# Performance work log

Hardware: AMD Instinct MI355X
Metric: run time of the kernel (lower is better)

The kernel has to match this reference:

```python
import jax, jax.numpy as jnp
import numpy as np

SOS = 1
V, H, B, T = 32000, 1024, 32, 64


def setup_inputs() -> dict:
    key = jax.random.key(0)
    ks = jax.random.split(key, 9)
    scale = 1.0 / np.sqrt(H)
    return {
        "encoder_outputs": jax.random.normal(ks[0], (B, T, H), dtype=jnp.float32),
        "encoder_hidden": jax.random.normal(ks[1], (1, B, H), dtype=jnp.float32),
        "target_tensor": jax.random.randint(ks[2], (B, T), 0, V),
        "embedding": jax.random.normal(ks[3], (V, H), dtype=jnp.float32),
        "w_ih": jax.random.uniform(ks[4], (3 * H, H), jnp.float32, -scale, scale),
        "w_hh": jax.random.uniform(ks[5], (3 * H, H), jnp.float32, -scale, scale),
        "b_ih": jax.random.uniform(ks[6], (3 * H,), jnp.float32, -scale, scale),
        "b_hh": jax.random.uniform(ks[7], (3 * H,), jnp.float32, -scale, scale),
        "w_out": jax.random.uniform(ks[8], (V, H), jnp.float32, -scale, scale),
        "b_out": jnp.zeros((V,), dtype=jnp.float32),
    }


def _gru_cell(x, h, w_ih, w_hh, b_ih, b_hh):
    # PyTorch GRU cell: gates ordered (r, z, n)
    gi = x @ w_ih.T + b_ih            # [B, 3H]
    gh = h @ w_hh.T + b_hh            # [B, 3H]
    i_r, i_z, i_n = jnp.split(gi, 3, axis=-1)
    h_r, h_z, h_n = jnp.split(gh, 3, axis=-1)
    r = jax.nn.sigmoid(i_r + h_r)
    z = jax.nn.sigmoid(i_z + h_z)
    n = jnp.tanh(i_n + r * h_n)
    return (1.0 - z) * n + z * h


def reference(encoder_outputs, encoder_hidden, target_tensor, embedding,
              w_ih, w_hh, b_ih, b_hh, w_out, b_out):
    batch = encoder_outputs.shape[0]
    # teacher-forced input tokens: [SOS, y_0, ..., y_{T-2}] -> [T, B]
    sos = jnp.full((batch, 1), SOS, dtype=target_tensor.dtype)
    tokens = jnp.concatenate([sos, target_tensor[:, :-1]], axis=1).T  # [T, B]

    h0 = encoder_hidden[0]  # [B, H]

    def step(h, tok):
        x = jax.nn.relu(embedding[tok])            # [B, H]
        h_new = _gru_cell(x, h, w_ih, w_hh, b_ih, b_hh)
        return h_new, h_new

    h_last, hs = jax.lax.scan(step, h0, tokens)    # hs: [T, B, H]
    logits = jnp.einsum('tbh,vh->btv', hs, w_out) + b_out  # [B, T, V]
    log_probs = jax.nn.log_softmax(logits, axis=-1)
    return log_probs, h_last[None]  # hidden returned as [1, B, H]
```

## Files before the change

### kernel.cpp

```cpp
#include <hip/hip_runtime.h>
#include <stdint.h>

#define Hd 1024
#define Bd 32
#define Td 64
#define Vd 32000
#define TB (Td*Bd)
#define G3H 3072
#define NB 64
#define JC 16
static const size_t BTV = (size_t)Bd * Td * Vd;

typedef unsigned short u16;
typedef __attribute__((ext_vector_type(8))) short bf16x8;
typedef __attribute__((ext_vector_type(4))) float f32x4;
typedef __attribute__((ext_vector_type(4))) unsigned int u32x4;

typedef __attribute__((address_space(3))) void lds_void;
typedef __attribute__((address_space(1))) const void gbl_void;

__device__ __forceinline__ void async_ld16(const void* g, void* l) {
    __builtin_amdgcn_global_load_lds((gbl_void*)g, (lds_void*)l, 16, 0, 0);
}

__device__ __forceinline__ u16 f2bf(float f) {
    union { float f; uint32_t u; } v; v.f = f;
    uint32_t u = v.u;
    return (u16)((u + 0x7fffu + ((u >> 16) & 1u)) >> 16);
}

__device__ __forceinline__ u32x4 gload_b128_sc(const u16* p) {
    u32x4 r;
    asm volatile("global_load_dwordx4 %0, %1, off sc0 sc1"
                 : "=v"(r) : "v"(p) : "memory");
    return r;
}
__device__ __forceinline__ void gstore_b32_sc(u16* p, unsigned int v) {
    asm volatile("global_store_dword %0, %1, off sc0 sc1"
                 :: "v"(p), "v"(v) : "memory");
}
__device__ __forceinline__ void gstore_u32_sc(unsigned int* p, unsigned int v) {
    asm volatile("global_store_dword %0, %1, off sc0 sc1"
                 :: "v"(p), "v"(v) : "memory");
}

__device__ __forceinline__ float fsigmoid(float x) {
    return __builtin_amdgcn_rcpf(1.f + __expf(-x));
}
__device__ __forceinline__ float ftanh(float x) {
    return 1.f - 2.f * __builtin_amdgcn_rcpf(1.f + __expf(2.f * x));
}

__global__ void k_conv_bf16(const float* __restrict__ src, u16* __restrict__ dst, int n4) {
    int i = blockIdx.x * blockDim.x + threadIdx.x;
    if (i >= n4) return;
    float4 f = ((const float4*)src)[i];
    ushort4 o;
    o.x = f2bf(f.x); o.y = f2bf(f.y); o.z = f2bf(f.z); o.w = f2bf(f.w);
    ((ushort4*)dst)[i] = o;
}

__global__ void k_embed(const float* __restrict__ emb, const int* __restrict__ tgt,
                        u16* __restrict__ Xb) {
    int r = blockIdx.x;
    int t = r >> 5, b = r & 31;
    int tok = (t == 0) ? 1 : tgt[b * Td + (t - 1)];
    const float4* srow = (const float4*)(emb + (size_t)tok * Hd);
    int k = threadIdx.x;
    float4 f = srow[k];
    ushort4 o;
    o.x = f2bf(fmaxf(f.x, 0.f)); o.y = f2bf(fmaxf(f.y, 0.f));
    o.z = f2bf(fmaxf(f.z, 0.f)); o.w = f2bf(fmaxf(f.w, 0.f));
    ((ushort4*)(Xb + (size_t)r * Hd))[k] = o;
}

__global__ void k_init_h(const float* __restrict__ eh, u16* __restrict__ hb,
                         unsigned int* __restrict__ cnt) {
    if (blockIdx.x == 0 && threadIdx.x < NB) cnt[threadIdx.x] = 0u;
    int i = blockIdx.x * blockDim.x + threadIdx.x;
    float4 f = ((const float4*)eh)[i];
    ushort4 o;
    o.x = f2bf(f.x); o.y = f2bf(f.y); o.z = f2bf(f.z); o.w = f2bf(f.w);
    ((ushort4*)hb)[i] = o;
}

template<int MODE, int SWAP>
__global__ __launch_bounds__(256, 2)
void k_gemm128(const u16* __restrict__ A, const u16* __restrict__ Bm,
               const float* __restrict__ bias, float* __restrict__ C,
               int N, int K)
{
    __shared__ alignas(16) u16 As[128 * 32];
    __shared__ alignas(16) u16 Bs[128 * 32];
    const int tid  = threadIdx.x;
    const int wave = tid >> 6;
    const int lane = tid & 63;
    const int l16  = lane & 15;
    const int q    = lane >> 4;
    const int wm   = (wave & 1) << 6;
    const int wn   = (wave >> 1) << 6;
    const int tm   = (SWAP ? blockIdx.x : blockIdx.y) << 7;
    const int tn   = (SWAP ? blockIdx.y : blockIdx.x) << 7;

    f32x4 acc[4][4];
#pragma unroll
    for (int i = 0; i < 4; ++i)
#pragma unroll
        for (int j = 0; j < 4; ++j) { f32x4 z = {0.f,0.f,0.f,0.f}; acc[i][j] = z; }

    const int c0 = wave * 2, c1 = wave * 2 + 1;
    const int cr = lane >> 2;
    const int kg = lane & 3;
    const u16* gA0 = A + (size_t)(tm + c0*16 + cr) * K + kg*8;
    const u16* gA1 = A + (size_t)(tm + c1*16 + cr) * K + kg*8;
    const u16* gB0 = Bm + (size_t)(tn + c0*16 + cr) * K + kg*8;
    const u16* gB1 = Bm + (size_t)(tn + c1*16 + cr) * K + kg*8;
    u16* lA0 = &As[c0*512 + lane*8];
    u16* lA1 = &As[c1*512 + lane*8];
    u16* lB0 = &Bs[c0*512 + lane*8];
    u16* lB1 = &Bs[c1*512 + lane*8];

    for (int k0 = 0; k0 < K; k0 += 32) {
        async_ld16(gA0 + k0, lA0);
        async_ld16(gA1 + k0, lA1);
        async_ld16(gB0 + k0, lB0);
        async_ld16(gB1 + k0, lB1);
        __syncthreads();
        bf16x8 af[4], bfr[4];
#pragma unroll
        for (int i = 0; i < 4; ++i)
            af[i] = *(const bf16x8*)&As[(wm + i*16 + l16) * 32 + q*8];
#pragma unroll
        for (int j = 0; j < 4; ++j)
            bfr[j] = *(const bf16x8*)&Bs[(wn + j*16 + l16) * 32 + q*8];
#pragma unroll
        for (int i = 0; i < 4; ++i)
#pragma unroll
            for (int j = 0; j < 4; ++j)
                acc[i][j] = __builtin_amdgcn_mfma_f32_16x16x32_bf16(af[i], bfr[j], acc[i][j], 0, 0, 0);
        __syncthreads();
    }

#pragma unroll
    for (int i = 0; i < 4; ++i) {
        const int mbase = tm + wm + i*16 + q*4;
#pragma unroll
        for (int j = 0; j < 4; ++j) {
            const int n = tn + wn + j*16 + l16;
            const float bv = bias[n];
#pragma unroll
            for (int r = 0; r < 4; ++r) {
                const int m = mbase + r;
                const float v = acc[i][j][r] + bv;
                if (MODE == 0) {
                    C[(size_t)m * N + n] = v;
                } else {
                    const int tt = m >> 5, bb = m & 31;
                    C[(size_t)((bb << 6) + tt) * Vd + n] = v;
                }
            }
        }
    }
}

__global__ __launch_bounds__(256, 1)
void k_gru_persist(const float* __restrict__ gi,
                   const float* __restrict__ enc_h,
                   const u16* __restrict__ w_hhb,
                   const float* __restrict__ b_hh,
                   u16* __restrict__ hbA, u16* __restrict__ hbB,
                   u16* __restrict__ hsb, float* __restrict__ hlast,
                   unsigned int* __restrict__ cnt)
{
    __shared__ alignas(16) u16 Ws[48 * 1024];
    __shared__ float ghs[2][3][32][17];
    const int tid = threadIdx.x;
    const int j0  = blockIdx.x * JC;

    for (int idx = tid; idx < 48 * 128; idx += 256) {
        int gr = idx >> 7;
        int c  = idx & 127;
        const u16* src = w_hhb + (size_t)((gr >> 4) * Hd + j0 + (gr & 15)) * Hd + c * 8;
        *(bf16x8*)&Ws[(size_t)(c * 48 + gr) * 8] = *(const bf16x8*)src;
    }

    const int b  = tid >> 3;
    const int jp = (tid & 7) * 2;
    float h0 = enc_h[b * Hd + j0 + jp];
    float h1 = enc_h[b * Hd + j0 + jp + 1];
    const float br0 = b_hh[j0 + jp],           br1 = b_hh[j0 + jp + 1];
    const float bz0 = b_hh[Hd + j0 + jp],      bz1 = b_hh[Hd + j0 + jp + 1];
    const float bn0 = b_hh[2*Hd + j0 + jp],    bn1 = b_hh[2*Hd + j0 + jp + 1];

    const int wave = tid >> 6, lane = tid & 63;
    const int l16 = lane & 15, q = lane >> 4;
    const int mh = wave & 1, kh = wave >> 1;

    float gr0, gr1, gz0, gz1, gn0, gn1;
    {
        const float* gir = gi + (size_t)b * G3H;
        gr0 = gir[j0 + jp];        gr1 = gir[j0 + jp + 1];
        gz0 = gir[Hd + j0 + jp];   gz1 = gir[Hd + j0 + jp + 1];
        gn0 = gir[2*Hd + j0 + jp]; gn1 = gir[2*Hd + j0 + jp + 1];
    }

    __syncthreads();

    for (int t = 0; t < Td; ++t) {
        const u16* hb_in  = (t & 1) ? hbB : hbA;
        u16*       hb_out = (t & 1) ? hbA : hbB;
        const int row = t * 32 + b;

        const u16* ap = hb_in + (size_t)(mh*16 + l16) * Hd + kh*512 + q*8;
        u32x4 areg[16];
#pragma unroll
        for (int it = 0; it < 16; ++it)
            areg[it] = gload_b128_sc(ap + it*32);

        asm volatile("s_waitcnt vmcnt(0)" ::: "memory");

        f32x4 acc0 = {0.f,0.f,0.f,0.f}, acc1 = acc0, acc2 = acc0;
#pragma unroll
        for (int it = 0; it < 16; ++it) {
            bf16x8 a = __builtin_bit_cast(bf16x8, areg[it]);
            const int kgrp = kh*64 + it*4 + q;
            const u16* wp = &Ws[(size_t)(kgrp * 48 + l16) * 8];
            bf16x8 w0 = *(const bf16x8*)(wp);
            bf16x8 w1 = *(const bf16x8*)(wp + 16*8);
            bf16x8 w2 = *(const bf16x8*)(wp + 32*8);
            acc0 = __builtin_amdgcn_mfma_f32_16x16x32_bf16(a, w0, acc0, 0, 0, 0);
            acc1 = __builtin_amdgcn_mfma_f32_16x16x32_bf16(a, w1, acc1, 0, 0, 0);
            acc2 = __builtin_amdgcn_mfma_f32_16x16x32_bf16(a, w2, acc2, 0, 0, 0);
        }
#pragma unroll
        for (int r = 0; r < 4; ++r) {
            const int bb = mh*16 + q*4 + r;
            ghs[kh][0][bb][l16] = acc0[r];
            ghs[kh][1][bb][l16] = acc1[r];
            ghs[kh][2][bb][l16] = acc2[r];
        }
        __syncthreads();

        {
            const float hr0 = ghs[0][0][b][jp]   + ghs[1][0][b][jp]   + br0;
            const float hr1 = ghs[0][0][b][jp+1] + ghs[1][0][b][jp+1] + br1;
            const float hz0 = ghs[0][1][b][jp]   + ghs[1][1][b][jp]   + bz0;
            const float hz1 = ghs[0][1][b][jp+1] + ghs[1][1][b][jp+1] + bz1;
            const float hn0 = ghs[0][2][b][jp]   + ghs[1][2][b][jp]   + bn0;
            const float hn1 = ghs[0][2][b][jp+1] + ghs[1][2][b][jp+1] + bn1;
            const float rg0 = fsigmoid(gr0 + hr0);
            const float rg1 = fsigmoid(gr1 + hr1);
            const float zg0 = fsigmoid(gz0 + hz0);
            const float zg1 = fsigmoid(gz1 + hz1);
            const float ng0 = ftanh(gn0 + rg0 * hn0);
            const float ng1 = ftanh(gn1 + rg1 * hn1);
            h0 = (1.f - zg0) * ng0 + zg0 * h0;
            h1 = (1.f - zg1) * ng1 + zg1 * h1;
            ushort2 pv; pv.x = f2bf(h0); pv.y = f2bf(h1);
            const unsigned int pw = (unsigned int)pv.x | ((unsigned int)pv.y << 16);
            gstore_b32_sc(&hb_out[b * Hd + j0 + jp], pw);
            *(ushort2*)&hsb[(size_t)row * Hd + j0 + jp] = pv;
            if (t == Td - 1) {
                hlast[b * Hd + j0 + jp]     = h0;
                hlast[b * Hd + j0 + jp + 1] = h1;
            }
        }

        if (t < Td - 1) {
            __syncthreads();
            if (tid == 0)
                gstore_u32_sc(&cnt[blockIdx.x], (unsigned)(t + 1));
            {
                const float* gir = gi + (size_t)((t + 1) * 32 + b) * G3H;
                gr0 = gir[j0 + jp];        gr1 = gir[j0 + jp + 1];
                gz0 = gir[Hd + j0 + jp];   gz1 = gir[Hd + j0 + jp + 1];
                gn0 = gir[2*Hd + j0 + jp]; gn1 = gir[2*Hd + j0 + jp + 1];
            }
            if (wave == 0) {
                const unsigned tgt = (unsigned)(t + 1);
                while (!__all(__hip_atomic_load(&cnt[lane], __ATOMIC_RELAXED,
                                                __HIP_MEMORY_SCOPE_AGENT) >= tgt))
                    __builtin_amdgcn_s_sleep(2);
            }
            __syncthreads();
        }
    }
}

__global__ __launch_bounds__(256)
void k_logsoftmax(float* __restrict__ out) {
    float* row = out + (size_t)blockIdx.x * Vd;
    const int tid = threadIdx.x;
    float m = -1e30f, s = 0.f;
    for (int i = tid * 4; i + 3 < Vd; i += 1024) {
        float4 f = *(const float4*)(row + i);
        float lm = fmaxf(fmaxf(f.x, f.y), fmaxf(f.z, f.w));
        if (lm > m) { s *= __expf(m - lm); m = lm; }
        s += __expf(f.x - m) + __expf(f.y - m) + __expf(f.z - m) + __expf(f.w - m);
    }
    for (int off = 32; off > 0; off >>= 1) {
        float mo = __shfl_down(m, off, 64);
        float so = __shfl_down(s, off, 64);
        float M = fmaxf(m, mo);
        s = s * __expf(m - M) + so * __expf(mo - M);
        m = M;
    }
    __shared__ float sm[4], ss[4];
    const int wave = tid >> 6, lane = tid & 63;
    if (lane == 0) { sm[wave] = m; ss[wave] = s; }
    __syncthreads();
    const float M = fmaxf(fmaxf(sm[0], sm[1]), fmaxf(sm[2], sm[3]));
    const float S = ss[0]*__expf(sm[0]-M) + ss[1]*__expf(sm[1]-M)
                  + ss[2]*__expf(sm[2]-M) + ss[3]*__expf(sm[3]-M);
    const float lz = M + logf(S);
    for (int i = tid * 4; i + 3 < Vd; i += 1024) {
        float4 f = *(const float4*)(row + i);
        f.x -= lz; f.y -= lz; f.z -= lz; f.w -= lz;
        *(float4*)(row + i) = f;
    }
}

extern "C" void kernel_launch(void* const* d_in, const int* in_sizes, int n_in,
                              void* d_out, int out_size, void* d_ws, size_t ws_size,
                              hipStream_t stream) {
    const float* enc_h = (const float*)d_in[1];
    const int*   tgt   = (const int*)d_in[2];
    const float* emb   = (const float*)d_in[3];
    const float* w_ih  = (const float*)d_in[4];
    const float* w_hh  = (const float*)d_in[5];
    const float* b_ih  = (const float*)d_in[6];
    const float* b_hh  = (const float*)d_in[7];
    const float* w_out = (const float*)d_in[8];
    const float* b_out = (const float*)d_in[9];
    float* out = (float*)d_out;

    char* ws = (char*)d_ws;
    size_t off = 0;
    auto alloc = [&](size_t bytes) { void* p = ws + off; off += (bytes + 255) & ~(size_t)255; return p; };
    u16*   w_outb = (u16*)  alloc((size_t)Vd * Hd * 2);
    u16*   w_ihb  = (u16*)  alloc((size_t)G3H * Hd * 2);
    u16*   w_hhb  = (u16*)  alloc((size_t)G3H * Hd * 2);
    u16*   Xb     = (u16*)  alloc((size_t)TB * Hd * 2);
    u16*   hsb    = (u16*)  alloc((size_t)TB * Hd * 2);
    float* gi     = (float*)alloc((size_t)TB * G3H * 4);
    u16*   hb0    = (u16*)  alloc((size_t)Bd * Hd * 2);
    u16*   hb1    = (u16*)  alloc((size_t)Bd * Hd * 2);
    unsigned int* cnt = (unsigned int*) alloc(256);
    (void)ws_size; (void)in_sizes; (void)n_in; (void)out_size;

    k_conv_bf16<<<(Vd*Hd/4 + 255)/256, 256, 0, stream>>>(w_out, w_outb, Vd*Hd/4);
    k_conv_bf16<<<(G3H*Hd/4 + 255)/256, 256, 0, stream>>>(w_ih, w_ihb, G3H*Hd/4);
    k_conv_bf16<<<(G3H*Hd/4 + 255)/256, 256, 0, stream>>>(w_hh, w_hhb, G3H*Hd/4);
    k_embed<<<TB, 256, 0, stream>>>(emb, tgt, Xb);
    k_init_h<<<32, 256, 0, stream>>>(enc_h, hb0, cnt);

    k_gemm128<0,0><<<dim3(G3H/128, TB/128), 256, 0, stream>>>(Xb, w_ihb, b_ih, gi, G3H, Hd);

    k_gru_persist<<<NB, 256, 0, stream>>>(gi, enc_h, w_hhb, b_hh, hb0, hb1, hsb,
                                          out + BTV, cnt);

    k_gemm128<1,1><<<dim3(TB/128, Vd/128), 256, 0, stream>>>(hsb, w_outb, b_out, out, Vd, Hd);

    k_logsoftmax<<<TB, 256, 0, stream>>>(out);
}
```

Before: 1.094 ms.

## Fuse GRU recurrence with output-projection GEMM in one persistent kernel

```diff
diff --git a/kernel.cpp b/kernel.cpp
--- a/kernel.cpp
+++ b/kernel.cpp
@@ -8,7 +8,9 @@
 #define TB (Td*Bd)
 #define G3H 3072
 #define NB 64
+#define NPOOL 192
 #define JC 16
+#define NTILE 250
 static const size_t BTV = (size_t)Bd * Td * Vd;
 
 typedef unsigned short u16;
@@ -164,125 +166,271 @@
 }
 
 __global__ __launch_bounds__(256, 1)
-void k_gru_persist(const float* __restrict__ gi,
-                   const float* __restrict__ enc_h,
-                   const u16* __restrict__ w_hhb,
-                   const float* __restrict__ b_hh,
-                   u16* __restrict__ hbA, u16* __restrict__ hbB,
-                   u16* __restrict__ hsb, float* __restrict__ hlast,
-                   unsigned int* __restrict__ cnt)
+void k_gru_logits(const float* __restrict__ gi,
+                  const float* __restrict__ enc_h,
+                  const u16* __restrict__ w_hhb,
+                  const float* __restrict__ b_hh,
+                  u16* __restrict__ hbA, u16* __restrict__ hbB,
+                  u16* __restrict__ hsb, float* __restrict__ hlast,
+                  unsigned int* __restrict__ cnt,
+                  const u16* __restrict__ w_outb,
+                  const float* __restrict__ b_out,
+                  float* __restrict__ out)
 {
-    __shared__ alignas(16) u16 Ws[48 * 1024];
-    __shared__ float ghs[2][3][32][17];
-    const int tid = threadIdx.x;
-    const int j0  = blockIdx.x * JC;
-
-    for (int idx = tid; idx < 48 * 128; idx += 256) {
-        int gr = idx >> 7;
-        int c  = idx & 127;
-        const u16* src = w_hhb + (size_t)((gr >> 4) * Hd + j0 + (gr & 15)) * Hd + c * 8;
-        *(bf16x8*)&Ws[(size_t)(c * 48 + gr) * 8] = *(const bf16x8*)src;
-    }
-
-    const int b  = tid >> 3;
-    const int jp = (tid & 7) * 2;
-    float h0 = enc_h[b * Hd + j0 + jp];
-    float h1 = enc_h[b * Hd + j0 + jp + 1];
-    const float br0 = b_hh[j0 + jp],           br1 = b_hh[j0 + jp + 1];
-    const float bz0 = b_hh[Hd + j0 + jp],      bz1 = b_hh[Hd + j0 + jp + 1];
-    const float bn0 = b_hh[2*Hd + j0 + jp],    bn1 = b_hh[2*Hd + j0 + jp + 1];
-
+    __shared__ alignas(16) unsigned char SM[111360];
+    const int tid  = threadIdx.x;
     const int wave = tid >> 6, lane = tid & 63;
-    const int l16 = lane & 15, q = lane >> 4;
-    const int mh = wave & 1, kh = wave >> 1;
-
-    float gr0, gr1, gz0, gz1, gn0, gn1;
-    {
-        const float* gir = gi + (size_t)b * G3H;
-        gr0 = gir[j0 + jp];        gr1 = gir[j0 + jp + 1];
-        gz0 = gir[Hd + j0 + jp];   gz1 = gir[Hd + j0 + jp + 1];
-        gn0 = gir[2*Hd + j0 + jp]; gn1 = gir[2*Hd + j0 + jp + 1];
-    }
-
-    __syncthreads();
-
-    for (int t = 0; t < Td; ++t) {
-        const u16* hb_in  = (t & 1) ? hbB : hbA;
-        u16*       hb_out = (t & 1) ? hbA : hbB;
-        const int row = t * 32 + b;
-
-        const u16* ap = hb_in + (size_t)(mh*16 + l16) * Hd + kh*512 + q*8;
-        u32x4 areg[16];
-#pragma unroll
-        for (int it = 0; it < 16; ++it)
-            areg[it] = gload_b128_sc(ap + it*32);
-
-        asm volatile("s_waitcnt vmcnt(0)" ::: "memory");
-
-        f32x4 acc0 = {0.f,0.f,0.f,0.f}, acc1 = acc0, acc2 = acc0;
-#pragma unroll
-        for (int it = 0; it < 16; ++it) {
-            bf16x8 a = __builtin_bit_cast(bf16x8, areg[it]);
-            const int kgrp = kh*64 + it*4 + q;
-            const u16* wp = &Ws[(size_t)(kgrp * 48 + l16) * 8];
-            bf16x8 w0 = *(const bf16x8*)(wp);
-            bf16x8 w1 = *(const bf16x8*)(wp + 16*8);
-            bf16x8 w2 = *(const bf16x8*)(wp + 32*8);
-            acc0 = __builtin_amdgcn_mfma_f32_16x16x32_bf16(a, w0, acc0, 0, 0, 0);
-            acc1 = __builtin_amdgcn_mfma_f32_16x16x32_bf16(a, w1, acc1, 0, 0, 0);
-            acc2 = __builtin_amdgcn_mfma_f32_16x16x32_bf16(a, w2, acc2, 0, 0, 0);
+    const int l16  = lane & 15, q = lane >> 4;
+
+    if (blockIdx.x < NB) {
+        u16* Ws = (u16*)SM;
+        typedef float ghs_t[3][32][17];
+        ghs_t* ghs = (ghs_t*)(SM + 98304);
+        const int j0 = blockIdx.x * JC;
+
+        for (int idx = tid; idx < 48 * 128; idx += 256) {
+            int gr = idx >> 7;
+            int c  = idx & 127;
+            const u16* src = w_hhb + (size_t)((gr >> 4) * Hd + j0 + (gr & 15)) * Hd + c * 8;
+            *(bf16x8*)&Ws[(size_t)(c * 48 + gr) * 8] = *(const bf16x8*)src;
         }
-#pragma unroll
-        for (int r = 0; r < 4; ++r) {
-            const int bb = mh*16 + q*4 + r;
-            ghs[kh][0][bb][l16] = acc0[r];
-            ghs[kh][1][bb][l16] = acc1[r];
-            ghs[kh][2][bb][l16] = acc2[r];
+
+        const int b  = tid >> 3;
+        const int jp = (tid & 7) * 2;
+        float h0 = enc_h[b * Hd + j0 + jp];
+        float h1 = enc_h[b * Hd + j0 + jp + 1];
+        const float br0 = b_hh[j0 + jp],           br1 = b_hh[j0 + jp + 1];
+        const float bz0 = b_hh[Hd + j0 + jp],      bz1 = b_hh[Hd + j0 + jp + 1];
+        const float bn0 = b_hh[2*Hd + j0 + jp],    bn1 = b_hh[2*Hd + j0 + jp + 1];
+
+        const int mh = wave & 1, kh = wave >> 1;
+
+        float gr0, gr1, gz0, gz1, gn0, gn1;
+        {
+            const float* gir = gi + (size_t)b * G3H;
+            gr0 = gir[j0 + jp];        gr1 = gir[j0 + jp + 1];
+            gz0 = gir[Hd + j0 + jp];   gz1 = gir[Hd + j0 + jp + 1];
+            gn0 = gir[2*Hd + j0 + jp]; gn1 = gir[2*Hd + j0 + jp + 1];
         }
+
         __syncthreads();
 
-        {
-            const float hr0 = ghs[0][0][b][jp]   + ghs[1][0][b][jp]   + br0;
-            const float hr1 = ghs[0][0][b][jp+1] + ghs[1][0][b][jp+1] + br1;
-            const float hz0 = ghs[0][1][b][jp]   + ghs[1][1][b][jp]   + bz0;
-            const float hz1 = ghs[0][1][b][jp+1] + ghs[1][1][b][jp+1] + bz1;
-            const float hn0 = ghs[0][2][b][jp]   + ghs[1][2][b][jp]   + bn0;
-            const float hn1 = ghs[0][2][b][jp+1] + ghs[1][2][b][jp+1] + bn1;
-            const float rg0 = fsigmoid(gr0 + hr0);
-            const float rg1 = fsigmoid(gr1 + hr1);
-            const float zg0 = fsigmoid(gz0 + hz0);
-            const float zg1 = fsigmoid(gz1 + hz1);
-            const float ng0 = ftanh(gn0 + rg0 * hn0);
-            const float ng1 = ftanh(gn1 + rg1 * hn1);
-            h0 = (1.f - zg0) * ng0 + zg0 * h0;
-            h1 = (1.f - zg1) * ng1 + zg1 * h1;
-            ushort2 pv; pv.x = f2bf(h0); pv.y = f2bf(h1);
-            const unsigned int pw = (unsigned int)pv.x | ((unsigned int)pv.y << 16);
-            gstore_b32_sc(&hb_out[b * Hd + j0 + jp], pw);
-            *(ushort2*)&hsb[(size_t)row * Hd + j0 + jp] = pv;
-            if (t == Td - 1) {
-                hlast[b * Hd + j0 + jp]     = h0;
-                hlast[b * Hd + j0 + jp + 1] = h1;
-            }
-        }
-
-        if (t < Td - 1) {
+        for (int t = 0; t < Td; ++t) {
+            const u16* hb_in  = (t & 1) ? hbB : hbA;
+            u16*       hb_out = (t & 1) ? hbA : hbB;
+            const int row = t * 32 + b;
+
+            const u16* ap = hb_in + (size_t)(mh*16 + l16) * Hd + kh*512 + q*8;
+            u32x4 areg[16];
+#pragma unroll
+            for (int it = 0; it < 16; ++it)
+                areg[it] = gload_b128_sc(ap + it*32);
+
+            asm volatile("s_waitcnt vmcnt(0)" ::: "memory");
+
+            f32x4 acc0 = {0.f,0.f,0.f,0.f}, acc1 = acc0, acc2 = acc0;
+#pragma unroll
+            for (int it = 0; it < 16; ++it) {
+                bf16x8 a = __builtin_bit_cast(bf16x8, areg[it]);
+                const int kgrp = kh*64 + it*4 + q;
+                const u16* wp = &Ws[(size_t)(kgrp * 48 + l16) * 8];
+                bf16x8 w0 = *(const bf16x8*)(wp);
+                bf16x8 w1 = *(const bf16x8*)(wp + 16*8);
+                bf16x8 w2 = *(const bf16x8*)(wp + 32*8);
+                acc0 = __builtin_amdgcn_mfma_f32_16x16x32_bf16(a, w0, acc0, 0, 0, 0);
+                acc1 = __builtin_amdgcn_mfma_f32_16x16x32_bf16(a, w1, acc1, 0, 0, 0);
+                acc2 = __builtin_amdgcn_mfma_f32_16x16x32_bf16(a, w2, acc2, 0, 0, 0);
+            }
+#pragma unroll
+            for (int r = 0; r < 4; ++r) {
+                const int bb = mh*16 + q*4 + r;
+                ghs[kh][0][bb][l16] = acc0[r];
+                ghs[kh][1][bb][l16] = acc1[r];
+                ghs[kh][2][bb][l16] = acc2[r];
+            }
+            __syncthreads();
+
+            {
+                const float hr0 = ghs[0][0][b][jp]   + ghs[1][0][b][jp]   + br0;
+                const float hr1 = ghs[0][0][b][jp+1] + ghs[1][0][b][jp+1] + br1;
+                const float hz0 = ghs[0][1][b][jp]   + ghs[1][1][b][jp]   + bz0;
+                const float hz1 = ghs[0][1][b][jp+1] + ghs[1][1][b][jp+1] + bz1;
+                const float hn0 = ghs[0][2][b][jp]   + ghs[1][2][b][jp]   + bn0;
+                const float hn1 = ghs[0][2][b][jp+1] + ghs[1][2][b][jp+1] + bn1;
+                const float rg0 = fsigmoid(gr0 + hr0);
+                const float rg1 = fsigmoid(gr1 + hr1);
+                const float zg0 = fsigmoid(gz0 + hz0);
+                const float zg1 = fsigmoid(gz1 + hz1);
+                const float ng0 = ftanh(gn0 + rg0 * hn0);
+                const float ng1 = ftanh(gn1 + rg1 * hn1);
+                h0 = (1.f - zg0) * ng0 + zg0 * h0;
+                h1 = (1.f - zg1) * ng1 + zg1 * h1;
+                ushort2 pv; pv.x = f2bf(h0); pv.y = f2bf(h1);
+                const unsigned int pw = (unsigned int)pv.x | ((unsigned int)pv.y << 16);
+                gstore_b32_sc(&hb_out[b * Hd + j0 + jp], pw);
+                gstore_b32_sc(&hsb[(size_t)row * Hd + j0 + jp], pw);
+                if (t == Td - 1) {
+                    hlast[b * Hd + j0 + jp]     = h0;
+                    hlast[b * Hd + j0 + jp + 1] = h1;
+                }
+            }
+
             __syncthreads();
             if (tid == 0)
                 gstore_u32_sc(&cnt[blockIdx.x], (unsigned)(t + 1));
-            {
-                const float* gir = gi + (size_t)((t + 1) * 32 + b) * G3H;
-                gr0 = gir[j0 + jp];        gr1 = gir[j0 + jp + 1];
-                gz0 = gir[Hd + j0 + jp];   gz1 = gir[Hd + j0 + jp + 1];
-                gn0 = gir[2*Hd + j0 + jp]; gn1 = gir[2*Hd + j0 + jp + 1];
-            }
+
+            if (t < Td - 1) {
+                {
+                    const float* gir = gi + (size_t)((t + 1) * 32 + b) * G3H;
+                    gr0 = gir[j0 + jp];        gr1 = gir[j0 + jp + 1];
+                    gz0 = gir[Hd + j0 + jp];   gz1 = gir[Hd + j0 + jp + 1];
+                    gn0 = gir[2*Hd + j0 + jp]; gn1 = gir[2*Hd + j0 + jp + 1];
+                }
+                if (wave == 0) {
+                    const unsigned tgt = (unsigned)(t + 1);
+                    while (!__all(__hip_atomic_load(&cnt[lane], __ATOMIC_RELAXED,
+                                                    __HIP_MEMORY_SCOPE_AGENT) >= tgt))
+                        __builtin_amdgcn_s_sleep(2);
+                }
+                __syncthreads();
+            }
+        }
+        return;
+    }
+
+    {
+        u16* As = (u16*)SM;
+        u16* Bs = (u16*)(SM + 32768);
+        const int g     = blockIdx.x - NB;
+        const int tile0 = g;
+        const int tile1 = g + NPOOL;
+        const bool two  = (tile1 < NTILE);
+
+        const int wm = (wave & 1) << 6;
+        const int wn = (wave >> 1) << 6;
+        const int c0 = wave * 2, c1 = wave * 2 + 1;
+        const int cr = lane >> 2;
+        const int kg = lane & 3;
+        const u16* gB0a = w_outb + (size_t)(tile0*128 + c0*16 + cr) * Hd + kg*8;
+        const u16* gB1a = w_outb + (size_t)(tile0*128 + c1*16 + cr) * Hd + kg*8;
+        const u16* gB0b = w_outb + (size_t)((two ? tile1 : tile0)*128 + c0*16 + cr) * Hd + kg*8;
+        const u16* gB1b = w_outb + (size_t)((two ? tile1 : tile0)*128 + c1*16 + cr) * Hd + kg*8;
+
+        const int arow  = tid >> 1;
+        const int ahalf = tid & 1;
+
+        for (int G = 0; G < 16; ++G) {
             if (wave == 0) {
-                const unsigned tgt = (unsigned)(t + 1);
+                const unsigned tgt = (unsigned)(4 * (G + 1));
                 while (!__all(__hip_atomic_load(&cnt[lane], __ATOMIC_RELAXED,
                                                 __HIP_MEMORY_SCOPE_AGENT) >= tgt))
-                    __builtin_amdgcn_s_sleep(2);
+                    __builtin_amdgcn_s_sleep(8);
             }
             __syncthreads();
+
+            f32x4 acc0[4][4], acc1[4][4];
+#pragma unroll
+            for (int i = 0; i < 4; ++i)
+#pragma unroll
+                for (int j = 0; j < 4; ++j) {
+                    f32x4 z = {0.f,0.f,0.f,0.f};
+                    acc0[i][j] = z; acc1[i][j] = z;
+                }
+
+            const size_t arow0 = (size_t)G * 128;
+
+            for (int s = 0; s < 8; ++s) {
+                const int k0 = s * 128;
+                const u16* asrc = hsb + (arow0 + arow) * Hd + k0 + ahalf * 64;
+                u32x4 ar[8];
+#pragma unroll
+                for (int j = 0; j < 8; ++j)
+                    ar[j] = gload_b128_sc(asrc + j*8);
+#pragma unroll
+                for (int kc = 0; kc < 4; ++kc) {
+                    const int kk = k0 + kc*32;
+                    u16* base0 = &Bs[(0*4 + kc) * 4096];
+                    async_ld16(gB0a + kk, base0 + c0*512 + lane*8);
+                    async_ld16(gB1a + kk, base0 + c1*512 + lane*8);
+                    if (two) {
+                        u16* base1 = &Bs[(1*4 + kc) * 4096];
+                        async_ld16(gB0b + kk, base1 + c0*512 + lane*8);
+                        async_ld16(gB1b + kk, base1 + c1*512 + lane*8);
+                    }
+                }
+                asm volatile("s_waitcnt vmcnt(0)" ::: "memory");
+#pragma unroll
+                for (int j = 0; j < 8; ++j) {
+                    const int ob = (ahalf*128 + j*16) ^ ((arow & 7) << 4);
+                    *(u32x4*)((unsigned char*)As + arow*256 + ob) = ar[j];
+                }
+                __syncthreads();
+
+#pragma unroll
+                for (int kc = 0; kc < 4; ++kc) {
+                    bf16x8 af[4];
+#pragma unroll
+                    for (int i = 0; i < 4; ++i) {
+                        const int row = wm + i*16 + l16;
+                        const int ob  = (kc*64 + q*16) ^ ((row & 7) << 4);
+                        af[i] = *(const bf16x8*)((const unsigned char*)As + row*256 + ob);
+                    }
+                    bf16x8 b0[4];
+#pragma unroll
+                    for (int j = 0; j < 4; ++j)
+                        b0[j] = *(const bf16x8*)&Bs[(0*4 + kc)*4096 + (wn + j*16 + l16)*32 + q*8];
+#pragma unroll
+                    for (int i = 0; i < 4; ++i)
+#pragma unroll
+                        for (int j = 0; j < 4; ++j)
+                            acc0[i][j] = __builtin_amdgcn_mfma_f32_16x16x32_bf16(af[i], b0[j], acc0[i][j], 0, 0, 0);
+                    if (two) {
+                        bf16x8 b1[4];
+#pragma unroll
+                        for (int j = 0; j < 4; ++j)
+                            b1[j] = *(const bf16x8*)&Bs[(1*4 + kc)*4096 + (wn + j*16 + l16)*32 + q*8];
+#pragma unroll
+                        for (int i = 0; i < 4; ++i)
+#pragma unroll
+                            for (int j = 0; j < 4; ++j)
+                                acc1[i][j] = __builtin_amdgcn_mfma_f32_16x16x32_bf16(af[i], b1[j], acc1[i][j], 0, 0, 0);
+                    }
+                }
+                __syncthreads();
+            }
+
+#pragma unroll
+            for (int i = 0; i < 4; ++i) {
+                const int lmbase = wm + i*16 + q*4;
+#pragma unroll
+                for (int j = 0; j < 4; ++j) {
+                    const int n0 = tile0*128 + wn + j*16 + l16;
+                    const float bv0 = b_out[n0];
+#pragma unroll
+                    for (int r = 0; r < 4; ++r) {
+                        const int gr = (int)(G*128) + lmbase + r;
+                        const int tt = gr >> 5, bb = gr & 31;
+                        out[(size_t)((bb << 6) + tt) * Vd + n0] = acc0[i][j][r] + bv0;
+                    }
+                }
+            }
+            if (two) {
+#pragma unroll
+                for (int i = 0; i < 4; ++i) {
+                    const int lmbase = wm + i*16 + q*4;
+#pragma unroll
+                    for (int j = 0; j < 4; ++j) {
+                        const int n1 = tile1*128 + wn + j*16 + l16;
+                        const float bv1 = b_out[n1];
+#pragma unroll
+                        for (int r = 0; r < 4; ++r) {
+                            const int gr = (int)(G*128) + lmbase + r;
+                            const int tt = gr >> 5, bb = gr & 31;
+                            out[(size_t)((bb << 6) + tt) * Vd + n1] = acc1[i][j][r] + bv1;
+                        }
+                    }
+                }
+            }
         }
     }
 }
@@ -356,10 +504,9 @@
 
     k_gemm128<0,0><<<dim3(G3H/128, TB/128), 256, 0, stream>>>(Xb, w_ihb, b_ih, gi, G3H, Hd);
 
-    k_gru_persist<<<NB, 256, 0, stream>>>(gi, enc_h, w_hhb, b_hh, hb0, hb1, hsb,
-                                          out + BTV, cnt);
-
-    k_gemm128<1,1><<<dim3(TB/128, Vd/128), 256, 0, stream>>>(hsb, w_outb, b_out, out, Vd, Hd);
+    k_gru_logits<<<NB + NPOOL, 256, 0, stream>>>(gi, enc_h, w_hhb, b_hh, hb0, hb1,
+                                                 hsb, out + BTV, cnt,
+                                                 w_outb, b_out, out);
 
     k_logsoftmax<<<TB, 256, 0, stream>>>(out);
 }
```

Result: slower. 1.186 ms (+8.4%).
